# Optimization experiments

Hardware: AMD Instinct MI355X
Metric: run time of the kernel (lower is better)

## Reference

```python
import jax, jax.numpy as jnp
import numpy as np

# config constants (match init_kwargs)
D_MODEL = 1024        # hidden_size
D_FF = 2048           # intermediate_size
N_EXPERTS = 8         # num_local_experts
TOP_K = 2             # num_experts_per_tok


def setup_inputs() -> dict:
    key = jax.random.key(0)
    k1, k2, k3, k4 = jax.random.split(key, 4)
    layer_input = jax.random.normal(k1, (2, 2048, D_MODEL), dtype=jnp.float32)
    # router: nn.Linear(hidden_size, num_experts, bias=False) -> weight [E, D]
    router_weight = jax.random.normal(k2, (N_EXPERTS, D_MODEL), dtype=jnp.float32) * 0.02
    # ParallelExperts weights: [num_experts, out_features, in_features]
    w_in = jax.random.normal(k3, (N_EXPERTS, 2 * D_FF, D_MODEL), dtype=jnp.float32) * 0.02
    w_out = jax.random.normal(k4, (N_EXPERTS, D_MODEL, D_FF), dtype=jnp.float32) * 0.02
    return {"layer_input": layer_input, "router_weight": router_weight,
            "w_in": w_in, "w_out": w_out}


def _moe_forward(x, router_weight, w_in, w_out):
    # x: [T, D]
    T = x.shape[0]
    logits = x @ router_weight.T                       # [T, E] router logits
    top_vals, top_idx = jax.lax.top_k(logits, TOP_K)   # [T, K]
    gates_k = jax.nn.softmax(top_vals, axis=-1).astype(x.dtype)
    # dense gate matrix: zero for unselected experts -> identical math to
    # the gather / grouped-GEMM / scatter-add path in the torch module.
    gates = jnp.zeros((T, N_EXPERTS), x.dtype).at[
        jnp.arange(T)[:, None], top_idx].set(gates_k)  # [T, E]
    # grouped GEMM #1: [E, T, 2*D_FF]
    h = jnp.einsum('td,efd->etf', x, w_in)
    h1, h2 = jnp.split(h, 2, axis=-1)
    act = jax.nn.silu(h1) * h2                         # SwiGLU: silu(a)*b
    # grouped GEMM #2: [E, T, D]
    y = jnp.einsum('eth,edh->etd', act, w_out)
    # gate-weighted combine (scatter-add equivalent)
    out = jnp.einsum('etd,te->td', y, gates)           # [T, D]
    return out, logits


def reference(layer_input, router_weight, w_in, w_out):
    bsz, length, emb = layer_input.shape
    x = layer_input.reshape(-1, emb)
    out, router_logits = _moe_forward(x, router_weight, w_in, w_out)
    return out.reshape(bsz, length, emb), router_logits
```

## Files before the change

### kernel.cpp

```cpp
#include <hip/hip_runtime.h>
#include <stdint.h>

#define N_TOK   4096
#define DMODEL  1024
#define DFF     2048
#define N_EXP   8
#define N_SLOTS (N_TOK * 2)
#define ROWS_PAD (N_SLOTS + 128)
#define MAX_TILES 72

typedef __bf16 bf16x8 __attribute__((ext_vector_type(8)));
typedef float  f32x4  __attribute__((ext_vector_type(4)));
typedef unsigned short u16;
typedef unsigned short u16x8 __attribute__((ext_vector_type(8)));
typedef unsigned short u16x4 __attribute__((ext_vector_type(4)));

__device__ __forceinline__ u16 f2bf(float f) {
    union { float f; uint32_t u; } v; v.f = f;
    uint32_t r = v.u + 0x7FFFu + ((v.u >> 16) & 1u);
    return (u16)(r >> 16);
}
__device__ __forceinline__ float bf2f(u16 u) {
    union { uint32_t u; float f; } v; v.u = ((uint32_t)u) << 16;
    return v.f;
}

__device__ __forceinline__ void g2l16(const void* gp, void* lp) {
    auto g = reinterpret_cast<const __attribute__((address_space(1))) unsigned int*>(
        reinterpret_cast<uintptr_t>(gp));
    auto l = reinterpret_cast<__attribute__((address_space(3))) unsigned int*>(
        reinterpret_cast<uintptr_t>(lp));
    __builtin_amdgcn_global_load_lds(g, l, 16, 0, 0);
}

__device__ __forceinline__ int idx64(int r, int cb) {
    return r * 64 + ((cb ^ (r & 7)) * 8);
}

#define CVT_BLOCKS 2048
#define CVT_THREADS (CVT_BLOCKS * 256)
#define NV4_WIN  (N_EXP * 2 * DFF * DMODEL / 4)
#define NV4_WOUT (N_EXP * DMODEL * DFF / 4)
#define RTR_BLOCKS (N_TOK / 4)

__global__ void cvt_router_kernel(const float4* __restrict__ win, const float4* __restrict__ wout,
                                  u16* __restrict__ winbf, u16* __restrict__ woutbf,
                                  const float* __restrict__ x, const float* __restrict__ rw,
                                  float* __restrict__ logits, int* __restrict__ tok_expert,
                                  float* __restrict__ tok_gate) {
    int bid = blockIdx.x;
    if (bid < CVT_BLOCKS) {
        int g = bid * 256 + threadIdx.x;
        u16x4* dwin  = (u16x4*)winbf;
        u16x4* dwout = (u16x4*)woutbf;
#pragma unroll 4
        for (int i = g; i < NV4_WIN; i += CVT_THREADS) {
            float4 a = win[i];
            u16x4 o = { f2bf(a.x), f2bf(a.y), f2bf(a.z), f2bf(a.w) };
            dwin[i] = o;
        }
#pragma unroll 4
        for (int i = g; i < NV4_WOUT; i += CVT_THREADS) {
            float4 a = wout[i];
            u16x4 o = { f2bf(a.x), f2bf(a.y), f2bf(a.z), f2bf(a.w) };
            dwout[i] = o;
        }
        return;
    }
    int t = (bid - CVT_BLOCKS) * 4 + (threadIdx.x >> 6);
    int lane = threadIdx.x & 63;
    const float* xr = x + (size_t)t * DMODEL;
    float acc[N_EXP];
#pragma unroll
    for (int e = 0; e < N_EXP; ++e) acc[e] = 0.f;
    for (int i = 0; i < DMODEL / 64; ++i) {
        int k = lane + i * 64;
        float xv = xr[k];
#pragma unroll
        for (int e = 0; e < N_EXP; ++e) acc[e] += xv * rw[e * DMODEL + k];
    }
#pragma unroll
    for (int e = 0; e < N_EXP; ++e) {
        float v = acc[e];
        for (int off = 32; off > 0; off >>= 1) v += __shfl_down(v, off, 64);
        acc[e] = v;
    }
    if (lane == 0) {
        float* lg = logits + (size_t)t * N_EXP;
#pragma unroll
        for (int e = 0; e < N_EXP; ++e) lg[e] = acc[e];
        int e0 = 0; float v0 = acc[0];
#pragma unroll
        for (int e = 1; e < N_EXP; ++e) if (acc[e] > v0) { v0 = acc[e]; e0 = e; }
        int e1 = -1; float v1 = -3.0e38f;
#pragma unroll
        for (int e = 0; e < N_EXP; ++e) if (e != e0 && acc[e] > v1) { v1 = acc[e]; e1 = e; }
        float ex = expf(v1 - v0);
        tok_expert[t * 2 + 0] = e0;  tok_gate[t * 2 + 0] = 1.0f / (1.0f + ex);
        tok_expert[t * 2 + 1] = e1;  tok_gate[t * 2 + 1] = ex / (1.0f + ex);
    }
}

__global__ void scan_kernel(const int* __restrict__ tok_expert, int* __restrict__ offs,
                            int* __restrict__ inv, int* __restrict__ tiletab) {
    __shared__ int cnt[N_EXP][257];
    __shared__ int soffs[N_EXP];
    int tid = threadIdx.x;
    int base = tid * 32;
    int loc[N_EXP];
#pragma unroll
    for (int e = 0; e < N_EXP; ++e) loc[e] = 0;
    for (int i = 0; i < 32; ++i) {
        int ex = tok_expert[base + i];
#pragma unroll
        for (int e = 0; e < N_EXP; ++e) loc[e] += (ex == e);
    }
#pragma unroll
    for (int e = 0; e < N_EXP; ++e) cnt[e][tid] = loc[e];
    __syncthreads();
    if (tid < N_EXP) {
        int running = 0;
        for (int t = 0; t < 256; ++t) { int c = cnt[tid][t]; cnt[tid][t] = running; running += c; }
        cnt[tid][256] = running;
    }
    __syncthreads();
    if (tid == 0) {
        int s = 0;
        for (int e = 0; e < N_EXP; ++e) { offs[e] = s; soffs[e] = s; s += cnt[e][256]; }
        offs[N_EXP] = s;
        int n = 0;
        for (int e = 0; e < N_EXP; ++e) {
            int c = cnt[e][256];
            int r0 = soffs[e];
            for (int m = 0; m * 128 < c; ++m) {
                int rem = c - m * 128;
                tiletab[4 + n * 4 + 0] = e;
                tiletab[4 + n * 4 + 1] = r0 + m * 128;
                tiletab[4 + n * 4 + 2] = rem < 128 ? rem : 128;
                ++n;
            }
        }
        tiletab[0] = n;
    }
    __syncthreads();
#pragma unroll
    for (int e = 0; e < N_EXP; ++e) loc[e] = 0;
    for (int i = 0; i < 32; ++i) {
        int ex = tok_expert[base + i];
        int row = 0;
#pragma unroll
        for (int e = 0; e < N_EXP; ++e)
            if (ex == e) { row = soffs[e] + cnt[e][tid] + loc[e]; loc[e]++; }
        inv[base + i] = row;
    }
}

__global__ void gather_kernel(const float* __restrict__ x, const int* __restrict__ inv,
                              u16* __restrict__ Abf) {
    int t = blockIdx.x;
    int r0 = inv[t * 2];
    int r1 = inv[t * 2 + 1];
    float4 v = ((const float4*)(x + (size_t)t * DMODEL))[threadIdx.x];
    u16x4 o = { f2bf(v.x), f2bf(v.y), f2bf(v.z), f2bf(v.w) };
    *(u16x4*)(Abf + (size_t)r0 * DMODEL + threadIdx.x * 4) = o;
    *(u16x4*)(Abf + (size_t)r1 * DMODEL + threadIdx.x * 4) = o;
}

__global__ __launch_bounds__(256, 4)
void gemm1_kernel(const u16* __restrict__ Abf, const u16* __restrict__ winbf,
                  u16* __restrict__ act, const int* __restrict__ tiletab) {
    int bid = blockIdx.x;
    int nt = bid & 31;
    int ti = bid >> 5;
    if (ti >= tiletab[0]) return;
    int e    = tiletab[4 + ti * 4 + 0];
    int row0 = tiletab[4 + ti * 4 + 1];
    int mmax = tiletab[4 + ti * 4 + 2];
    int n0 = nt * 64;
    const u16* wb = winbf + (size_t)e * (2 * DFF) * DMODEL;

    __shared__ u16 lsA[128 * 64];
    __shared__ u16 lsB[2][64 * 64];

    int tid = threadIdx.x, lane = tid & 63, wave = tid >> 6;
    int wm = wave >> 1, wn = wave & 1;
    int s_r8 = lane >> 3;
    int s_cb = ((lane & 7) ^ (lane >> 3)) * 8;

    f32x4 acc[2][4][2];
    f32x4 zero = {0.f, 0.f, 0.f, 0.f};
#pragma unroll
    for (int h = 0; h < 2; ++h)
#pragma unroll
        for (int mi = 0; mi < 4; ++mi)
#pragma unroll
            for (int ni = 0; ni < 2; ++ni) acc[h][mi][ni] = zero;

    for (int kk = 0; kk < DMODEL / 64; ++kk) {
        int k0 = kk * 64;
#pragma unroll
        for (int q = 0; q < 4; ++q) {
            int R0 = wave * 32 + q * 8;
            g2l16(Abf + (size_t)(row0 + R0 + s_r8) * DMODEL + k0 + s_cb, &lsA[R0 * 64]);
        }
#pragma unroll
        for (int h = 0; h < 2; ++h)
#pragma unroll
            for (int q = 0; q < 2; ++q) {
                int R0 = wave * 16 + q * 8;
                g2l16(wb + (size_t)(h * DFF + n0 + R0 + s_r8) * DMODEL + k0 + s_cb,
                      &lsB[h][R0 * 64]);
            }
        __syncthreads();
#pragma unroll
        for (int kh = 0; kh < 2; ++kh) {
            int cb = kh * 4 + (lane >> 4);
            bf16x8 afr[4];
#pragma unroll
            for (int mi = 0; mi < 4; ++mi)
                afr[mi] = *(const bf16x8*)&lsA[idx64(wm * 64 + mi * 16 + (lane & 15), cb)];
#pragma unroll
            for (int h = 0; h < 2; ++h)
#pragma unroll
                for (int ni = 0; ni < 2; ++ni) {
                    bf16x8 bfr = *(const bf16x8*)&lsB[h][idx64(wn * 32 + ni * 16 + (lane & 15), cb)];
#pragma unroll
                    for (int mi = 0; mi < 4; ++mi)
                        acc[h][mi][ni] = __builtin_amdgcn_mfma_f32_16x16x32_bf16(
                            afr[mi], bfr, acc[h][mi][ni], 0, 0, 0);
                }
        }
        __syncthreads();
    }
#pragma unroll
    for (int mi = 0; mi < 4; ++mi)
#pragma unroll
        for (int i = 0; i < 4; ++i) {
            int rl = wm * 64 + mi * 16 + (lane >> 4) * 4 + i;
            if (rl < mmax) {
                size_t rp = (size_t)(row0 + rl) * DFF;
#pragma unroll
                for (int ni = 0; ni < 2; ++ni) {
                    int col = n0 + wn * 32 + ni * 16 + (lane & 15);
                    float a = acc[0][mi][ni][i];
                    float b = acc[1][mi][ni][i];
                    float sv = a / (1.0f + __expf(-a));
                    act[rp + col] = f2bf(sv * b);
                }
            }
        }
}

__global__ __launch_bounds__(256, 4)
void gemm2_kernel(const u16* __restrict__ act, const u16* __restrict__ woutbf,
                  u16* __restrict__ ybA, u16* __restrict__ ybB,
                  const int* __restrict__ tiletab) {
    int bid = blockIdx.x;
    int kc = bid & 1;
    int nt = (bid >> 1) & 7;
    int ti = bid >> 4;
    if (ti >= tiletab[0]) return;
    int e    = tiletab[4 + ti * 4 + 0];
    int row0 = tiletab[4 + ti * 4 + 1];
    int mmax = tiletab[4 + ti * 4 + 2];
    int n0 = nt * 128;
    const u16* wb = woutbf + (size_t)e * DMODEL * DFF;

    __shared__ u16 lsA[128 * 64];
    __shared__ u16 lsB[128 * 64];

    int tid = threadIdx.x, lane = tid & 63, wave = tid >> 6;
    int wm = wave >> 1, wn = wave & 1;
    int s_r8 = lane >> 3;
    int s_cb = ((lane & 7) ^ (lane >> 3)) * 8;
    u16* yb = kc ? ybB : ybA;

    f32x4 acc[4][4];
    f32x4 zero = {0.f, 0.f, 0.f, 0.f};
#pragma unroll
    for (int mi = 0; mi < 4; ++mi)
#pragma unroll
        for (int ni = 0; ni < 4; ++ni) acc[mi][ni] = zero;

    for (int kk = kc * 16; kk < kc * 16 + 16; ++kk) {
        int k0 = kk * 64;
#pragma unroll
        for (int q = 0; q < 4; ++q) {
            int R0 = wave * 32 + q * 8;
            g2l16(act + (size_t)(row0 + R0 + s_r8) * DFF + k0 + s_cb, &lsA[R0 * 64]);
            g2l16(wb + (size_t)(n0 + R0 + s_r8) * DFF + k0 + s_cb, &lsB[R0 * 64]);
        }
        __syncthreads();
#pragma unroll
        for (int kh = 0; kh < 2; ++kh) {
            int cb = kh * 4 + (lane >> 4);
            bf16x8 afr[4];
#pragma unroll
            for (int mi = 0; mi < 4; ++mi)
                afr[mi] = *(const bf16x8*)&lsA[idx64(wm * 64 + mi * 16 + (lane & 15), cb)];
#pragma unroll
            for (int ni = 0; ni < 4; ++ni) {
                bf16x8 bfr = *(const bf16x8*)&lsB[idx64(wn * 64 + ni * 16 + (lane & 15), cb)];
#pragma unroll
                for (int mi = 0; mi < 4; ++mi)
                    acc[mi][ni] = __builtin_amdgcn_mfma_f32_16x16x32_bf16(
                        afr[mi], bfr, acc[mi][ni], 0, 0, 0);
            }
        }
        __syncthreads();
    }
#pragma unroll
    for (int mi = 0; mi < 4; ++mi)
#pragma unroll
        for (int i = 0; i < 4; ++i) {
            int rl = wm * 64 + mi * 16 + (lane >> 4) * 4 + i;
            if (rl < mmax) {
                u16* yrow = yb + (size_t)(row0 + rl) * DMODEL;
#pragma unroll
                for (int ni = 0; ni < 4; ++ni) {
                    int col = n0 + wn * 64 + ni * 16 + (lane & 15);
                    yrow[col] = f2bf(acc[mi][ni][i]);
                }
            }
        }
}

__global__ void combine_kernel(const u16* __restrict__ ybA, const u16* __restrict__ ybB,
                               const int* __restrict__ inv, const float* __restrict__ tok_gate,
                               float* __restrict__ out) {
    int t = blockIdx.x;
    int tid = threadIdx.x;
    __shared__ int sr0, sr1;
    __shared__ float sg0, sg1;
    if (tid == 0) {
        sr0 = inv[t * 2];  sr1 = inv[t * 2 + 1];
        sg0 = tok_gate[t * 2];  sg1 = tok_gate[t * 2 + 1];
    }
    __syncthreads();
    int d = tid * 4;
    u16x4 a0 = *(const u16x4*)(ybA + (size_t)sr0 * DMODEL + d);
    u16x4 b0 = *(const u16x4*)(ybB + (size_t)sr0 * DMODEL + d);
    u16x4 a1 = *(const u16x4*)(ybA + (size_t)sr1 * DMODEL + d);
    u16x4 b1 = *(const u16x4*)(ybB + (size_t)sr1 * DMODEL + d);
    float4 o;
    o.x = sg0 * (bf2f(a0.x) + bf2f(b0.x)) + sg1 * (bf2f(a1.x) + bf2f(b1.x));
    o.y = sg0 * (bf2f(a0.y) + bf2f(b0.y)) + sg1 * (bf2f(a1.y) + bf2f(b1.y));
    o.z = sg0 * (bf2f(a0.z) + bf2f(b0.z)) + sg1 * (bf2f(a1.z) + bf2f(b1.z));
    o.w = sg0 * (bf2f(a0.w) + bf2f(b0.w)) + sg1 * (bf2f(a1.w) + bf2f(b1.w));
    *(float4*)(out + (size_t)t * DMODEL + d) = o;
}

extern "C" void kernel_launch(void* const* d_in, const int* in_sizes, int n_in,
                              void* d_out, int out_size, void* d_ws, size_t ws_size,
                              hipStream_t stream) {
    const float* x    = (const float*)d_in[0];
    const float* rw   = (const float*)d_in[1];
    const float* win  = (const float*)d_in[2];
    const float* wout = (const float*)d_in[3];
    float* out    = (float*)d_out;
    float* logits = out + (size_t)N_TOK * DMODEL;

    char* ws = (char*)d_ws;
    size_t o = 0;
    auto alloc = [&](size_t bytes) -> void* {
        void* p = ws + o;
        o = (o + bytes + 255) & ~(size_t)255;
        return p;
    };
    u16*   Abf      = (u16*)  alloc((size_t)ROWS_PAD * DMODEL * 2);
    u16*   actbuf   = (u16*)  alloc((size_t)ROWS_PAD * DFF * 2);
    u16*   winbf    = (u16*)  alloc((size_t)N_EXP * 2 * DFF * DMODEL * 2);
    u16*   woutbf   = (u16*)  alloc((size_t)N_EXP * DMODEL * DFF * 2);
    int*   offs     = (int*)  alloc(16 * 4);
    int*   inv      = (int*)  alloc(N_SLOTS * 4);
    int*   tok_exp  = (int*)  alloc(N_SLOTS * 4);
    float* tok_gate = (float*)alloc(N_SLOTS * 4);
    int*   tiletab  = (int*)  alloc((4 + MAX_TILES * 4) * 4);
    u16*   ybA      = winbf;
    u16*   ybB      = winbf + (size_t)ROWS_PAD * DMODEL;
    (void)ws_size; (void)in_sizes; (void)n_in; (void)out_size;

    cvt_router_kernel<<<CVT_BLOCKS + RTR_BLOCKS, 256, 0, stream>>>(
        (const float4*)win, (const float4*)wout, winbf, woutbf,
        x, rw, logits, tok_exp, tok_gate);
    scan_kernel<<<1, 256, 0, stream>>>(tok_exp, offs, inv, tiletab);
    gather_kernel<<<N_TOK, 256, 0, stream>>>(x, inv, Abf);
    gemm1_kernel<<<MAX_TILES * 32, 256, 0, stream>>>(Abf, winbf, actbuf, tiletab);
    gemm2_kernel<<<MAX_TILES * 16, 256, 0, stream>>>(actbuf, woutbf, ybA, ybB, tiletab);
    combine_kernel<<<N_TOK, 256, 0, stream>>>(ybA, ybB, inv, tok_gate, out);
}
```

Baseline: 449.6 us.

## Split weight conversion across later kernels to overlap with gather and GEMM1

The fp32-to-bf16 conversion of w_in now rides as extra blocks in the gather kernel, and the conversion of w_out rides as extra blocks appended to the GEMM1 grid. Before, both conversions ran in the router kernel. The aim is to hide conversion bandwidth behind the gather and GEMM1 work instead of running it up front. GEMM1 blocks now compete with the conversion blocks for CUs and memory bandwidth, so GEMM1 could slow down if the GEMM blocks are not scheduled first.

New measurement: 428.8 us. -4.6%, faster.

```diff
diff --git a/kernel.cpp b/kernel.cpp
--- a/kernel.cpp
+++ b/kernel.cpp
@@ -12,7 +12,6 @@
 typedef __bf16 bf16x8 __attribute__((ext_vector_type(8)));
 typedef float  f32x4  __attribute__((ext_vector_type(4)));
 typedef unsigned short u16;
-typedef unsigned short u16x8 __attribute__((ext_vector_type(8)));
 typedef unsigned short u16x4 __attribute__((ext_vector_type(4)));
 
 __device__ __forceinline__ u16 f2bf(float f) {
@@ -37,37 +36,19 @@
     return r * 64 + ((cb ^ (r & 7)) * 8);
 }
 
-#define CVT_BLOCKS 2048
-#define CVT_THREADS (CVT_BLOCKS * 256)
+#define RTR_BLOCKS (N_TOK / 4)
+#define WCVT1_BLOCKS 2048
+#define WCVT1_THREADS (WCVT1_BLOCKS * 256)
 #define NV4_WIN  (N_EXP * 2 * DFF * DMODEL / 4)
+#define WCVT2_BLOCKS 1024
+#define WCVT2_THREADS (WCVT2_BLOCKS * 256)
 #define NV4_WOUT (N_EXP * DMODEL * DFF / 4)
-#define RTR_BLOCKS (N_TOK / 4)
-
-__global__ void cvt_router_kernel(const float4* __restrict__ win, const float4* __restrict__ wout,
-                                  u16* __restrict__ winbf, u16* __restrict__ woutbf,
-                                  const float* __restrict__ x, const float* __restrict__ rw,
-                                  float* __restrict__ logits, int* __restrict__ tok_expert,
-                                  float* __restrict__ tok_gate) {
-    int bid = blockIdx.x;
-    if (bid < CVT_BLOCKS) {
-        int g = bid * 256 + threadIdx.x;
-        u16x4* dwin  = (u16x4*)winbf;
-        u16x4* dwout = (u16x4*)woutbf;
-#pragma unroll 4
-        for (int i = g; i < NV4_WIN; i += CVT_THREADS) {
-            float4 a = win[i];
-            u16x4 o = { f2bf(a.x), f2bf(a.y), f2bf(a.z), f2bf(a.w) };
-            dwin[i] = o;
-        }
-#pragma unroll 4
-        for (int i = g; i < NV4_WOUT; i += CVT_THREADS) {
-            float4 a = wout[i];
-            u16x4 o = { f2bf(a.x), f2bf(a.y), f2bf(a.z), f2bf(a.w) };
-            dwout[i] = o;
-        }
-        return;
-    }
-    int t = (bid - CVT_BLOCKS) * 4 + (threadIdx.x >> 6);
+#define GEMM1_GRID (MAX_TILES * 32)
+
+__global__ void router_kernel(const float* __restrict__ x, const float* __restrict__ rw,
+                              float* __restrict__ logits, int* __restrict__ tok_expert,
+                              float* __restrict__ tok_gate) {
+    int t = blockIdx.x * 4 + (threadIdx.x >> 6);
     int lane = threadIdx.x & 63;
     const float* xr = x + (size_t)t * DMODEL;
     float acc[N_EXP];
@@ -155,21 +136,44 @@
     }
 }
 
-__global__ void gather_kernel(const float* __restrict__ x, const int* __restrict__ inv,
-                              u16* __restrict__ Abf) {
-    int t = blockIdx.x;
-    int r0 = inv[t * 2];
-    int r1 = inv[t * 2 + 1];
-    float4 v = ((const float4*)(x + (size_t)t * DMODEL))[threadIdx.x];
-    u16x4 o = { f2bf(v.x), f2bf(v.y), f2bf(v.z), f2bf(v.w) };
-    *(u16x4*)(Abf + (size_t)r0 * DMODEL + threadIdx.x * 4) = o;
-    *(u16x4*)(Abf + (size_t)r1 * DMODEL + threadIdx.x * 4) = o;
+__global__ void gather_cvt_kernel(const float* __restrict__ x, const int* __restrict__ inv,
+                                  u16* __restrict__ Abf,
+                                  const float4* __restrict__ win, u16x4* __restrict__ winbf4) {
+    int bid = blockIdx.x;
+    if (bid < N_TOK) {
+        int t = bid;
+        int r0 = inv[t * 2];
+        int r1 = inv[t * 2 + 1];
+        float4 v = ((const float4*)(x + (size_t)t * DMODEL))[threadIdx.x];
+        u16x4 o = { f2bf(v.x), f2bf(v.y), f2bf(v.z), f2bf(v.w) };
+        *(u16x4*)(Abf + (size_t)r0 * DMODEL + threadIdx.x * 4) = o;
+        *(u16x4*)(Abf + (size_t)r1 * DMODEL + threadIdx.x * 4) = o;
+        return;
+    }
+    int g = (bid - N_TOK) * 256 + threadIdx.x;
+#pragma unroll 4
+    for (int i = g; i < NV4_WIN; i += WCVT1_THREADS) {
+        float4 a = win[i];
+        u16x4 o = { f2bf(a.x), f2bf(a.y), f2bf(a.z), f2bf(a.w) };
+        winbf4[i] = o;
+    }
 }
 
 __global__ __launch_bounds__(256, 4)
 void gemm1_kernel(const u16* __restrict__ Abf, const u16* __restrict__ winbf,
-                  u16* __restrict__ act, const int* __restrict__ tiletab) {
+                  u16* __restrict__ act, const int* __restrict__ tiletab,
+                  const float4* __restrict__ wout, u16x4* __restrict__ woutbf4) {
     int bid = blockIdx.x;
+    if (bid >= GEMM1_GRID) {
+        int g = (bid - GEMM1_GRID) * 256 + threadIdx.x;
+#pragma unroll 4
+        for (int i = g; i < NV4_WOUT; i += WCVT2_THREADS) {
+            float4 a = wout[i];
+            u16x4 o = { f2bf(a.x), f2bf(a.y), f2bf(a.z), f2bf(a.w) };
+            woutbf4[i] = o;
+        }
+        return;
+    }
     int nt = bid & 31;
     int ti = bid >> 5;
     if (ti >= tiletab[0]) return;
@@ -380,12 +384,12 @@
     u16*   ybB      = winbf + (size_t)ROWS_PAD * DMODEL;
     (void)ws_size; (void)in_sizes; (void)n_in; (void)out_size;
 
-    cvt_router_kernel<<<CVT_BLOCKS + RTR_BLOCKS, 256, 0, stream>>>(
-        (const float4*)win, (const float4*)wout, winbf, woutbf,
-        x, rw, logits, tok_exp, tok_gate);
+    router_kernel<<<RTR_BLOCKS, 256, 0, stream>>>(x, rw, logits, tok_exp, tok_gate);
     scan_kernel<<<1, 256, 0, stream>>>(tok_exp, offs, inv, tiletab);
-    gather_kernel<<<N_TOK, 256, 0, stream>>>(x, inv, Abf);
-    gemm1_kernel<<<MAX_TILES * 32, 256, 0, stream>>>(Abf, winbf, actbuf, tiletab);
+    gather_cvt_kernel<<<N_TOK + WCVT1_BLOCKS, 256, 0, stream>>>(
+        x, inv, Abf, (const float4*)win, (u16x4*)winbf);
+    gemm1_kernel<<<GEMM1_GRID + WCVT2_BLOCKS, 256, 0, stream>>>(
+        Abf, winbf, actbuf, tiletab, (const float4*)wout, (u16x4*)woutbf);
     gemm2_kernel<<<MAX_TILES * 16, 256, 0, stream>>>(actbuf, woutbf, ybA, ybB, tiletab);
     combine_kernel<<<N_TOK, 256, 0, stream>>>(ybA, ybB, inv, tok_gate, out);
 }
```
